# Kernel tuning notes

Measured on AMD Instinct MI355X. Metric: run time of the kernel, lower is better.

The kernel has to match this reference:

```python
import jax, jax.numpy as jnp
import numpy as np

N_NODES = 100000
N_EDGES = 1600000
D = 128            # in_size == d_model == 128
N_LAYERS = 4
N_GRAPHS = 64
N_CLASS = 10
BN_EPS = 1e-5


def setup_inputs() -> dict:
    key = jax.random.key(0)
    ks = jax.random.split(key, 20)
    x = jax.random.normal(ks[0], (N_NODES, D), dtype=jnp.float32)
    edge_index = jax.random.randint(ks[1], (2, N_EDGES), 0, N_NODES, dtype=jnp.int32)
    batch = jnp.sort(jax.random.randint(ks[2], (N_NODES,), 0, N_GRAPHS, dtype=jnp.int32))
    s = 0.05
    # stacked per-layer GINConv MLP params (all layers are D->D since in_size==d_model)
    W1 = jax.random.normal(ks[3], (N_LAYERS, D, D), dtype=jnp.float32) * s
    b1 = jnp.zeros((N_LAYERS, D), dtype=jnp.float32)
    W2 = jax.random.normal(ks[4], (N_LAYERS, D, D), dtype=jnp.float32) * s
    b2 = jnp.zeros((N_LAYERS, D), dtype=jnp.float32)
    gamma = jnp.ones((N_LAYERS, D), dtype=jnp.float32)
    beta = jnp.zeros((N_LAYERS, D), dtype=jnp.float32)
    eps = jnp.zeros((N_LAYERS,), dtype=jnp.float32)  # train_eps=True, init 0
    fcw1 = jax.random.normal(ks[5], (D, D), dtype=jnp.float32) * s
    fcb1 = jnp.zeros((D,), dtype=jnp.float32)
    fcw2 = jax.random.normal(ks[6], (D, D // 2), dtype=jnp.float32) * s
    fcb2 = jnp.zeros((D // 2,), dtype=jnp.float32)
    fcw3 = jax.random.normal(ks[7], (D // 2, N_CLASS), dtype=jnp.float32) * s
    fcb3 = jnp.zeros((N_CLASS,), dtype=jnp.float32)
    return dict(x=x, edge_index=edge_index, batch=batch, W1=W1, b1=b1, W2=W2, b2=b2,
                gamma=gamma, beta=beta, eps=eps, fcw1=fcw1, fcb1=fcb1,
                fcw2=fcw2, fcb2=fcb2, fcw3=fcw3, fcb3=fcb3)


def _batchnorm(z, g, b):
    # BatchNorm1d in training mode: batch stats over nodes, biased variance
    m = jnp.mean(z, axis=0)
    v = jnp.var(z, axis=0)
    return g * (z - m) * jax.lax.rsqrt(v + BN_EPS) + b


def reference(x, edge_index, batch, W1, b1, W2, b2, gamma, beta, eps,
              fcw1, fcb1, fcw2, fcb2, fcw3, fcb3):
    # StandardScaler: per-feature standardization over all nodes (ddof=0)
    mu = jnp.mean(x, axis=0)
    sd = jnp.sqrt(jnp.var(x, axis=0))
    h = (x - mu) / sd
    src, dst = edge_index[0], edge_index[1]
    for l in range(N_LAYERS):
        # GINConv: MLP((1+eps)*x_i + sum_{j in N(i)} x_j)
        agg = jax.ops.segment_sum(h[src], dst, num_segments=N_NODES)
        z = (1.0 + eps[l]) * h + agg
        z = jax.nn.relu(z @ W1[l] + b1[l])
        z = jax.nn.relu(z @ W2[l] + b2[l])
        z = _batchnorm(z, gamma[l], beta[l])
        h = jax.nn.relu(z)  # outer F.relu in forward
    g = jax.ops.segment_sum(h, batch, num_segments=N_GRAPHS)  # global_add_pool
    g = jax.nn.relu(g @ fcw1 + fcb1)   # dropout omitted (eval/deterministic)
    g = jax.nn.relu(g @ fcw2 + fcb2)
    return g @ fcw3 + fcb3
```

## Files before the change

kernel.cpp:

```cpp
#include <hip/hip_runtime.h>
#include <hip/hip_bf16.h>
#include <math.h>

#define N_NODES 100000
#define N_EDGES 1600000
#define D 128
#define N_LAYERS 4
#define N_GRAPHS 64
#define N_CLASS 10
#define BN_EPS 1e-5f

#define POOL_ROWS 128
#define LDK 136

#define EB_CHUNK 4096
#define EDGE_BLOCKS ((N_EDGES + EB_CHUNK - 1) / EB_CHUNK)
#define NPB 512
#define NB ((N_NODES + NPB - 1) / NPB)

typedef __attribute__((ext_vector_type(8))) short bf16x8;
typedef __attribute__((ext_vector_type(4))) float f32x4;

__device__ inline float b2f(ushort u) {
    return __builtin_bit_cast(float, (unsigned)u << 16);
}
__device__ inline ushort f2b(float f) {
    unsigned u = __builtin_bit_cast(unsigned, f);
    return (ushort)((u + 0x7fffu + ((u >> 16) & 1u)) >> 16);
}

__global__ void prep_all_kernel(float* __restrict__ statsAll, float* __restrict__ ab,
                                float* __restrict__ gpool, int* __restrict__ bucketCount) {
    int t = threadIdx.x;
    for (int i = t; i < 10 * D; i += 1024) statsAll[i] = 0.f;
    if (t < D) { ab[t] = 1.f; ab[D + t] = 0.f; }
    for (int i = t; i < N_GRAPHS * D; i += 1024) gpool[i] = 0.f;
    for (int i = t; i < NB; i += 1024) bucketCount[i] = 0;
}

__global__ void bucket_count_kernel(const int* __restrict__ dst, int* __restrict__ bucketCount) {
    __shared__ int bc[NB];
    int tid = threadIdx.x;
    if (tid < NB) bc[tid] = 0;
    __syncthreads();
    int base = blockIdx.x * EB_CHUNK;
#pragma unroll
    for (int i = 0; i < 16; ++i) {
        int e = base + i * 256 + tid;
        if (e < N_EDGES) atomicAdd(&bc[dst[e] >> 9], 1);
    }
    __syncthreads();
    if (tid < NB && bc[tid]) atomicAdd(&bucketCount[tid], bc[tid]);
}

__global__ void bucket_scan_kernel(const int* __restrict__ bucketCount,
                                   int* __restrict__ bucketBase, int* __restrict__ bucketCursor) {
    __shared__ int lds[256];
    int tid = threadIdx.x;
    int v = (tid < NB) ? bucketCount[tid] : 0;
    lds[tid] = v;
    __syncthreads();
    for (int off = 1; off < 256; off <<= 1) {
        int x = (tid >= off) ? lds[tid - off] : 0;
        __syncthreads();
        lds[tid] += x;
        __syncthreads();
    }
    int excl = lds[tid] - v;
    if (tid < NB) { bucketBase[tid] = excl; bucketCursor[tid] = excl; }
    if (tid == NB - 1) bucketBase[NB] = excl + v;
}

__global__ void bucket_scatter_kernel(const int* __restrict__ src, const int* __restrict__ dst,
                                      int* __restrict__ bucketCursor, int2* __restrict__ bpairs) {
    __shared__ int lcnt[NB];
    int tid = threadIdx.x;
    if (tid < NB) lcnt[tid] = 0;
    __syncthreads();
    int base = blockIdx.x * EB_CHUNK;
    int s[16], d[16];
#pragma unroll
    for (int i = 0; i < 16; ++i) {
        int e = base + i * 256 + tid;
        if (e < N_EDGES) {
            s[i] = src[e]; d[i] = dst[e];
            atomicAdd(&lcnt[d[i] >> 9], 1);
        } else {
            d[i] = -1;
        }
    }
    __syncthreads();
    if (tid < NB) {
        int c = lcnt[tid];
        lcnt[tid] = c ? atomicAdd(&bucketCursor[tid], c) : 0;
    }
    __syncthreads();
#pragma unroll
    for (int i = 0; i < 16; ++i) {
        if (d[i] >= 0) {
            int p = atomicAdd(&lcnt[d[i] >> 9], 1);
            bpairs[p] = make_int2(s[i], d[i]);
        }
    }
}

__launch_bounds__(512)
__global__ void csr_build_kernel(const int2* __restrict__ bpairs, const int* __restrict__ bucketBase,
                                 int* __restrict__ rowptr, int* __restrict__ colidx) {
    __shared__ int cnt[NPB];
    __shared__ int cur[NPB];
    int tid = threadIdx.x;
    int b = blockIdx.x;
    int nb0 = b * NPB;
    int ebase = bucketBase[b];
    int eend = bucketBase[b + 1];
    cnt[tid] = 0;
    __syncthreads();
    for (int e = ebase + tid; e < eend; e += 512)
        atomicAdd(&cnt[bpairs[e].y - nb0], 1);
    __syncthreads();
    int v = cnt[tid];
    for (int off = 1; off < 512; off <<= 1) {
        int x = (tid >= off) ? cnt[tid - off] : 0;
        __syncthreads();
        cnt[tid] += x;
        __syncthreads();
    }
    int excl = cnt[tid] - v;
    int node = nb0 + tid;
    if (node < N_NODES) rowptr[node] = ebase + excl;
    cur[tid] = ebase + excl;
    __syncthreads();
    for (int e = ebase + tid; e < eend; e += 512) {
        int2 pr = bpairs[e];
        int p = atomicAdd(&cur[pr.y - nb0], 1);
        colidx[p] = pr.x;
    }
    if (b == 0 && tid == 0) rowptr[N_NODES] = N_EDGES;
}

__global__ void colstats_kernel(const float* __restrict__ x, float* __restrict__ stats) {
    __shared__ float ssum[D];
    __shared__ float ssq[D];
    int tid = threadIdx.x;
    if (tid < D) { ssum[tid] = 0.f; ssq[tid] = 0.f; }
    __syncthreads();
    int f4 = (tid & 31) * 4;
    int rsub = tid >> 5;
    int r0 = blockIdx.x * 128;
    int rend = r0 + 128;
    if (rend > N_NODES) rend = N_NODES;
    float4 ps = make_float4(0.f, 0.f, 0.f, 0.f);
    float4 pq = make_float4(0.f, 0.f, 0.f, 0.f);
    for (int r = r0 + rsub; r < rend; r += 8) {
        float4 v = *(const float4*)&x[(size_t)r * D + f4];
        ps.x += v.x; ps.y += v.y; ps.z += v.z; ps.w += v.w;
        pq.x += v.x * v.x; pq.y += v.y * v.y; pq.z += v.z * v.z; pq.w += v.w * v.w;
    }
    atomicAdd(&ssum[f4 + 0], ps.x); atomicAdd(&ssum[f4 + 1], ps.y);
    atomicAdd(&ssum[f4 + 2], ps.z); atomicAdd(&ssum[f4 + 3], ps.w);
    atomicAdd(&ssq[f4 + 0], pq.x);  atomicAdd(&ssq[f4 + 1], pq.y);
    atomicAdd(&ssq[f4 + 2], pq.z);  atomicAdd(&ssq[f4 + 3], pq.w);
    __syncthreads();
    if (tid < D) {
        atomicAdd(&stats[tid], ssum[tid]);
        atomicAdd(&stats[D + tid], ssq[tid]);
    }
}

__global__ void standardize_kernel(const float* __restrict__ x, const float* __restrict__ stats,
                                   ushort* __restrict__ h) {
    const float invN = 1.f / (float)N_NODES;
    int stride = gridDim.x * blockDim.x;
    const int total = N_NODES * (D / 4);
    for (int idx = blockIdx.x * blockDim.x + threadIdx.x; idx < total; idx += stride) {
        int f = (idx & 31) * 4;
        float4 v = ((const float4*)x)[idx];
        float o[4];
        float vv[4] = {v.x, v.y, v.z, v.w};
#pragma unroll
        for (int j = 0; j < 4; ++j) {
            float mu = stats[f + j] * invN;
            float sd = sqrtf(stats[D + f + j] * invN - mu * mu);
            o[j] = (vv[j] - mu) / sd;
        }
        ((ushort4*)h)[idx] = make_ushort4(f2b(o[0]), f2b(o[1]), f2b(o[2]), f2b(o[3]));
    }
}

__global__ void agg_kernel(const ushort* __restrict__ h, const int* __restrict__ rowptr,
                           const int* __restrict__ colidx, const float* __restrict__ eps, int l,
                           const float* __restrict__ ab, int relu_flag,
                           ushort* __restrict__ z0) {
    int node = blockIdx.x * 8 + (threadIdx.x >> 5);
    int f4 = (threadIdx.x & 31) * 4;
    const ushort* hp = h + f4;
    float A0 = ab[f4 + 0], A1 = ab[f4 + 1], A2 = ab[f4 + 2], A3 = ab[f4 + 3];
    float B0 = ab[D + f4 + 0], B1 = ab[D + f4 + 1], B2 = ab[D + f4 + 2], B3 = ab[D + f4 + 3];
    float lo = relu_flag ? 0.f : -INFINITY;
    auto R0 = [&](ushort u) { return fmaxf(fmaf(b2f(u), A0, B0), lo); };
    auto R1 = [&](ushort u) { return fmaxf(fmaf(b2f(u), A1, B1), lo); };
    auto R2 = [&](ushort u) { return fmaxf(fmaf(b2f(u), A2, B2), lo); };
    auto R3 = [&](ushort u) { return fmaxf(fmaf(b2f(u), A3, B3), lo); };

    ushort4 c = *(const ushort4*)&hp[(size_t)node * D];
    float se = 1.f + eps[l];
    float ax = se * R0(c.x), ay = se * R1(c.y), az = se * R2(c.z), aw = se * R3(c.w);

    int e = rowptr[node], e1 = rowptr[node + 1];
    for (; e + 4 <= e1; e += 4) {
        int s0 = colidx[e], s1 = colidx[e + 1], s2 = colidx[e + 2], s3 = colidx[e + 3];
        ushort4 v0 = *(const ushort4*)&hp[(size_t)s0 * D];
        ushort4 v1 = *(const ushort4*)&hp[(size_t)s1 * D];
        ushort4 v2 = *(const ushort4*)&hp[(size_t)s2 * D];
        ushort4 v3 = *(const ushort4*)&hp[(size_t)s3 * D];
        ax += (R0(v0.x) + R0(v1.x)) + (R0(v2.x) + R0(v3.x));
        ay += (R1(v0.y) + R1(v1.y)) + (R1(v2.y) + R1(v3.y));
        az += (R2(v0.z) + R2(v1.z)) + (R2(v2.z) + R2(v3.z));
        aw += (R3(v0.w) + R3(v1.w)) + (R3(v2.w) + R3(v3.w));
    }
    for (; e < e1; ++e) {
        ushort4 v0 = *(const ushort4*)&hp[(size_t)colidx[e] * D];
        ax += R0(v0.x); ay += R1(v0.y); az += R2(v0.z); aw += R3(v0.w);
    }
    *(ushort4*)&z0[(size_t)node * D + f4] = make_ushort4(f2b(ax), f2b(ay), f2b(az), f2b(aw));
}

__global__ void prep_wt_kernel(const float* __restrict__ W1, const float* __restrict__ W2,
                               ushort* __restrict__ wt) {
    int idx = blockIdx.x * blockDim.x + threadIdx.x;
    int w = idx >> 16;
    int rem = idx & 65535;
    int l = rem >> 14;
    int nk = rem & 16383;
    int n = nk >> 7;
    int k = nk & 127;
    const float* W = w ? W2 : W1;
    wt[idx] = f2b(W[((size_t)(l * D + k)) * D + n]);
}

__launch_bounds__(256, 4)
__global__ void mlp_mfma_kernel(const ushort* __restrict__ z0,
                                const ushort* __restrict__ wt1, const float* __restrict__ b1,
                                const ushort* __restrict__ wt2, const float* __restrict__ b2,
                                ushort* __restrict__ out, float* __restrict__ stats) {
    __shared__ ushort Z[128 * LDK];
    __shared__ float Ssum[D];
    __shared__ float Ssq[D];

    int tid = threadIdx.x;
    int lane = tid & 63;
    int wave = tid >> 6;
    int rb = blockIdx.x * 128;
    int lrow = lane & 15;
    int lk = lane >> 4;
    int klane = lk * 8;
    int wr0 = wave * 32;

    if (tid < D) { Ssum[tid] = 0.f; Ssq[tid] = 0.f; }

    bf16x8 zero8;
#pragma unroll
    for (int e = 0; e < 8; ++e) zero8[e] = 0;

    int ra0 = rb + wr0 + lrow;
    int ra1 = ra0 + 16;
    bool ok0 = ra0 < N_NODES;
    bool ok1 = ra1 < N_NODES;
    const ushort* pa0 = z0 + (size_t)ra0 * D + klane;
    const ushort* pa1 = z0 + (size_t)ra1 * D + klane;
    const ushort* pb1 = wt1 + (size_t)lrow * D + klane;
    const ushort* pb2 = wt2 + (size_t)lrow * D + klane;

    f32x4 acc[2][8];
#pragma unroll
    for (int a = 0; a < 2; ++a)
#pragma unroll
        for (int b = 0; b < 8; ++b)
#pragma unroll
            for (int r = 0; r < 4; ++r) acc[a][b][r] = 0.f;

#pragma unroll
    for (int ks = 0; ks < 4; ++ks) {
        bf16x8 a0 = ok0 ? *(const bf16x8*)(pa0 + ks * 32) : zero8;
        bf16x8 a1 = ok1 ? *(const bf16x8*)(pa1 + ks * 32) : zero8;
#pragma unroll
        for (int ct = 0; ct < 8; ++ct) {
            bf16x8 bb = *(const bf16x8*)(pb1 + (size_t)ct * 16 * D + ks * 32);
            acc[0][ct] = __builtin_amdgcn_mfma_f32_16x16x32_bf16(a0, bb, acc[0][ct], 0, 0, 0);
            acc[1][ct] = __builtin_amdgcn_mfma_f32_16x16x32_bf16(a1, bb, acc[1][ct], 0, 0, 0);
        }
    }

#pragma unroll
    for (int rt = 0; rt < 2; ++rt)
#pragma unroll
        for (int ct = 0; ct < 8; ++ct) {
            int col = ct * 16 + lrow;
            float bias = b1[col];
#pragma unroll
            for (int r = 0; r < 4; ++r) {
                int row = wr0 + rt * 16 + lk * 4 + r;
                Z[row * LDK + col] = f2b(fmaxf(acc[rt][ct][r] + bias, 0.f));
            }
        }

#pragma unroll
    for (int a = 0; a < 2; ++a)
#pragma unroll
        for (int b = 0; b < 8; ++b)
#pragma unroll
            for (int r = 0; r < 4; ++r) acc[a][b][r] = 0.f;

#pragma unroll
    for (int ks = 0; ks < 4; ++ks) {
        int k0 = ks * 32 + klane;
        bf16x8 a0 = *(const bf16x8*)&Z[(wr0 + lrow) * LDK + k0];
        bf16x8 a1 = *(const bf16x8*)&Z[(wr0 + 16 + lrow) * LDK + k0];
#pragma unroll
        for (int ct = 0; ct < 8; ++ct) {
            bf16x8 bb = *(const bf16x8*)(pb2 + (size_t)ct * 16 * D + ks * 32);
            acc[0][ct] = __builtin_amdgcn_mfma_f32_16x16x32_bf16(a0, bb, acc[0][ct], 0, 0, 0);
            acc[1][ct] = __builtin_amdgcn_mfma_f32_16x16x32_bf16(a1, bb, acc[1][ct], 0, 0, 0);
        }
    }

    float ls[8], lq[8];
#pragma unroll
    for (int ct = 0; ct < 8; ++ct) { ls[ct] = 0.f; lq[ct] = 0.f; }
#pragma unroll
    for (int rt = 0; rt < 2; ++rt)
#pragma unroll
        for (int ct = 0; ct < 8; ++ct) {
            int col = ct * 16 + lrow;
            float bias = b2[col];
#pragma unroll
            for (int r = 0; r < 4; ++r) {
                int row = wr0 + rt * 16 + lk * 4 + r;
                float v = fmaxf(acc[rt][ct][r] + bias, 0.f);
                Z[row * LDK + col] = f2b(v);
                if (rb + row < N_NODES) { ls[ct] += v; lq[ct] += v * v; }
            }
        }
    __syncthreads();

#pragma unroll
    for (int ct = 0; ct < 8; ++ct) {
        int col = ct * 16 + lrow;
        atomicAdd(&Ssum[col], ls[ct]);
        atomicAdd(&Ssq[col], lq[ct]);
    }

#pragma unroll
    for (int i = 0; i < 8; ++i) {
        int c2 = tid + i * 256;
        int row = c2 >> 4;
        int cc = (c2 & 15) * 8;
        int gr = rb + row;
        if (gr < N_NODES)
            *(bf16x8*)&out[(size_t)gr * D + cc] = *(const bf16x8*)&Z[row * LDK + cc];
    }
    __syncthreads();
    if (tid < D) {
        atomicAdd(&stats[tid], Ssum[tid]);
        atomicAdd(&stats[D + tid], Ssq[tid]);
    }
}

__global__ void bnprep_kernel(const float* __restrict__ stats, const float* __restrict__ gamma,
                              const float* __restrict__ beta, float* __restrict__ ab) {
    int f = threadIdx.x;
    if (f < D) {
        const float invN = 1.f / (float)N_NODES;
        float mu = stats[f] * invN;
        float var = stats[D + f] * invN - mu * mu;
        float A = gamma[f] * rsqrtf(var + BN_EPS);
        ab[f] = A;
        ab[D + f] = beta[f] - mu * A;
    }
}

__global__ void pool_kernel(const ushort* __restrict__ h, const int* __restrict__ batch,
                            const float* __restrict__ ab, float* __restrict__ g) {
    int tid = threadIdx.x;
    int f4 = (tid & 31) * 4;
    int rsub = tid >> 5;
    int r0 = blockIdx.x * POOL_ROWS;
    int rend = r0 + POOL_ROWS;
    if (rend > N_NODES) rend = N_NODES;
    float A0 = ab[f4 + 0], A1 = ab[f4 + 1], A2 = ab[f4 + 2], A3 = ab[f4 + 3];
    float B0 = ab[D + f4 + 0], B1 = ab[D + f4 + 1], B2 = ab[D + f4 + 2], B3 = ab[D + f4 + 3];
    float4 acc = make_float4(0.f, 0.f, 0.f, 0.f);
    int cur = -1;
    for (int r = r0 + rsub; r < rend; r += 8) {
        int b = batch[r];
        if (b != cur) {
            if (cur >= 0) {
                atomicAdd(&g[cur * D + f4 + 0], acc.x);
                atomicAdd(&g[cur * D + f4 + 1], acc.y);
                atomicAdd(&g[cur * D + f4 + 2], acc.z);
                atomicAdd(&g[cur * D + f4 + 3], acc.w);
            }
            acc = make_float4(0.f, 0.f, 0.f, 0.f);
            cur = b;
        }
        ushort4 v = *(const ushort4*)&h[(size_t)r * D + f4];
        acc.x += fmaxf(fmaf(b2f(v.x), A0, B0), 0.f);
        acc.y += fmaxf(fmaf(b2f(v.y), A1, B1), 0.f);
        acc.z += fmaxf(fmaf(b2f(v.z), A2, B2), 0.f);
        acc.w += fmaxf(fmaf(b2f(v.w), A3, B3), 0.f);
    }
    if (cur >= 0) {
        atomicAdd(&g[cur * D + f4 + 0], acc.x);
        atomicAdd(&g[cur * D + f4 + 1], acc.y);
        atomicAdd(&g[cur * D + f4 + 2], acc.z);
        atomicAdd(&g[cur * D + f4 + 3], acc.w);
    }
}

__launch_bounds__(512)
__global__ void head_kernel(const float* __restrict__ g,
                            const float* __restrict__ fcw1, const float* __restrict__ fcb1,
                            const float* __restrict__ fcw2, const float* __restrict__ fcb2,
                            const float* __restrict__ fcw3, const float* __restrict__ fcb3,
                            float* __restrict__ out) {
    __shared__ float G[64][128];
    __shared__ float T1[64][128];
    __shared__ float T2[64][64];
    int tid = threadIdx.x;
#pragma unroll
    for (int i = 0; i < 4; ++i) {
        int slot = tid + i * 512;
        ((float4*)G)[slot] = ((const float4*)g)[slot];
    }
    __syncthreads();
#pragma unroll 1
    for (int rep = 0; rep < 16; ++rep) {
        int o = tid + rep * 512;
        int r = o >> 7, c = o & 127;
        float acc = fcb1[c];
        for (int k = 0; k < 128; ++k) acc = fmaf(G[r][k], fcw1[k * 128 + c], acc);
        T1[r][c] = fmaxf(acc, 0.f);
    }
    __syncthreads();
#pragma unroll 1
    for (int rep = 0; rep < 8; ++rep) {
        int o = tid + rep * 512;
        int r = o >> 6, c = o & 63;
        float acc = fcb2[c];
        for (int k = 0; k < 128; ++k) acc = fmaf(T1[r][k], fcw2[k * 64 + c], acc);
        T2[r][c] = fmaxf(acc, 0.f);
    }
    __syncthreads();
    for (int o = tid; o < N_GRAPHS * N_CLASS; o += 512) {
        int r = o / 10, c = o % 10;
        float acc = fcb3[c];
        for (int k = 0; k < 64; ++k) acc = fmaf(T2[r][k], fcw3[k * 10 + c], acc);
        out[o] = acc;
    }
}

extern "C" void kernel_launch(void* const* d_in, const int* in_sizes, int n_in,
                              void* d_out, int out_size, void* d_ws, size_t ws_size,
                              hipStream_t stream) {
    const float* x        = (const float*)d_in[0];
    const int* edge_index = (const int*)d_in[1];
    const int* batch      = (const int*)d_in[2];
    const float* W1       = (const float*)d_in[3];
    const float* b1       = (const float*)d_in[4];
    const float* W2       = (const float*)d_in[5];
    const float* b2       = (const float*)d_in[6];
    const float* gamma    = (const float*)d_in[7];
    const float* beta     = (const float*)d_in[8];
    const float* eps      = (const float*)d_in[9];
    const float* fcw1     = (const float*)d_in[10];
    const float* fcb1     = (const float*)d_in[11];
    const float* fcw2     = (const float*)d_in[12];
    const float* fcb2     = (const float*)d_in[13];
    const float* fcw3     = (const float*)d_in[14];
    const float* fcb3     = (const float*)d_in[15];
    float* out = (float*)d_out;

    char* ws = (char*)d_ws;
    size_t off = 0;
    auto alloc = [&](size_t bytes) -> void* {
        void* p = ws + off;
        off = (off + bytes + 255) & ~(size_t)255;
        return p;
    };
    ushort* hbuf   = (ushort*)alloc((size_t)N_NODES * D * 2);
    ushort* z0buf  = (ushort*)alloc((size_t)N_NODES * D * 2);
    ushort* wtbuf  = (ushort*)alloc((size_t)2 * N_LAYERS * D * D * 2);
    int2* bpairs   = (int2*)alloc((size_t)N_EDGES * 8);
    int* colidx    = (int*)alloc((size_t)N_EDGES * 4);
    int* rowptr    = (int*)alloc((size_t)(N_NODES + 1) * 4);
    int* bucketCount  = (int*)alloc((size_t)NB * 4);
    int* bucketBase   = (int*)alloc((size_t)(NB + 1) * 4);
    int* bucketCursor = (int*)alloc((size_t)NB * 4);
    float* statsAll = (float*)alloc(12 * D * 4);
    float* gpool   = (float*)alloc((size_t)N_GRAPHS * D * 4);
    float* scalerStats = statsAll + 8 * D;
    float* ab          = statsAll + 10 * D;

    const int* srcArr = edge_index;
    const int* dstArr = edge_index + N_EDGES;

    prep_all_kernel<<<1, 1024, 0, stream>>>(statsAll, ab, gpool, bucketCount);

    bucket_count_kernel<<<EDGE_BLOCKS, 256, 0, stream>>>(dstArr, bucketCount);
    bucket_scan_kernel<<<1, 256, 0, stream>>>(bucketCount, bucketBase, bucketCursor);
    bucket_scatter_kernel<<<EDGE_BLOCKS, 256, 0, stream>>>(srcArr, dstArr, bucketCursor, bpairs);
    csr_build_kernel<<<NB, 512, 0, stream>>>(bpairs, bucketBase, rowptr, colidx);

    colstats_kernel<<<(N_NODES + 127) / 128, 256, 0, stream>>>(x, scalerStats);
    standardize_kernel<<<2048, 256, 0, stream>>>(x, scalerStats, hbuf);

    prep_wt_kernel<<<512, 256, 0, stream>>>(W1, W2, wtbuf);

    for (int l = 0; l < N_LAYERS; ++l) {
        float* lstats = statsAll + (size_t)l * 2 * D;
        agg_kernel<<<N_NODES / 8, 256, 0, stream>>>(hbuf, rowptr, colidx, eps, l,
                                                    ab, (l > 0) ? 1 : 0, z0buf);
        mlp_mfma_kernel<<<(N_NODES + 127) / 128, 256, 0, stream>>>(
            z0buf, wtbuf + (size_t)l * D * D, b1 + (size_t)l * D,
            wtbuf + (size_t)(N_LAYERS + l) * D * D, b2 + (size_t)l * D, hbuf, lstats);
        bnprep_kernel<<<1, 128, 0, stream>>>(lstats, gamma + (size_t)l * D,
                                             beta + (size_t)l * D, ab);
    }

    pool_kernel<<<(N_NODES + POOL_ROWS - 1) / POOL_ROWS, 256, 0, stream>>>(hbuf, batch, ab, gpool);
    head_kernel<<<1, 512, 0, stream>>>(gpool, fcw1, fcb1, fcw2, fcb2, fcw3, fcb3, out);
}
```

Baseline: 788.3 us.

## Fuse neighbor aggregation into MLP kernel via shared-memory staging and ping-pong buffers

```diff
diff --git a/kernel.cpp b/kernel.cpp
--- a/kernel.cpp
+++ b/kernel.cpp
@@ -188,44 +188,6 @@
     }
 }
 
-__global__ void agg_kernel(const ushort* __restrict__ h, const int* __restrict__ rowptr,
-                           const int* __restrict__ colidx, const float* __restrict__ eps, int l,
-                           const float* __restrict__ ab, int relu_flag,
-                           ushort* __restrict__ z0) {
-    int node = blockIdx.x * 8 + (threadIdx.x >> 5);
-    int f4 = (threadIdx.x & 31) * 4;
-    const ushort* hp = h + f4;
-    float A0 = ab[f4 + 0], A1 = ab[f4 + 1], A2 = ab[f4 + 2], A3 = ab[f4 + 3];
-    float B0 = ab[D + f4 + 0], B1 = ab[D + f4 + 1], B2 = ab[D + f4 + 2], B3 = ab[D + f4 + 3];
-    float lo = relu_flag ? 0.f : -INFINITY;
-    auto R0 = [&](ushort u) { return fmaxf(fmaf(b2f(u), A0, B0), lo); };
-    auto R1 = [&](ushort u) { return fmaxf(fmaf(b2f(u), A1, B1), lo); };
-    auto R2 = [&](ushort u) { return fmaxf(fmaf(b2f(u), A2, B2), lo); };
-    auto R3 = [&](ushort u) { return fmaxf(fmaf(b2f(u), A3, B3), lo); };
-
-    ushort4 c = *(const ushort4*)&hp[(size_t)node * D];
-    float se = 1.f + eps[l];
-    float ax = se * R0(c.x), ay = se * R1(c.y), az = se * R2(c.z), aw = se * R3(c.w);
-
-    int e = rowptr[node], e1 = rowptr[node + 1];
-    for (; e + 4 <= e1; e += 4) {
-        int s0 = colidx[e], s1 = colidx[e + 1], s2 = colidx[e + 2], s3 = colidx[e + 3];
-        ushort4 v0 = *(const ushort4*)&hp[(size_t)s0 * D];
-        ushort4 v1 = *(const ushort4*)&hp[(size_t)s1 * D];
-        ushort4 v2 = *(const ushort4*)&hp[(size_t)s2 * D];
-        ushort4 v3 = *(const ushort4*)&hp[(size_t)s3 * D];
-        ax += (R0(v0.x) + R0(v1.x)) + (R0(v2.x) + R0(v3.x));
-        ay += (R1(v0.y) + R1(v1.y)) + (R1(v2.y) + R1(v3.y));
-        az += (R2(v0.z) + R2(v1.z)) + (R2(v2.z) + R2(v3.z));
-        aw += (R3(v0.w) + R3(v1.w)) + (R3(v2.w) + R3(v3.w));
-    }
-    for (; e < e1; ++e) {
-        ushort4 v0 = *(const ushort4*)&hp[(size_t)colidx[e] * D];
-        ax += R0(v0.x); ay += R1(v0.y); az += R2(v0.z); aw += R3(v0.w);
-    }
-    *(ushort4*)&z0[(size_t)node * D + f4] = make_ushort4(f2b(ax), f2b(ay), f2b(az), f2b(aw));
-}
-
 __global__ void prep_wt_kernel(const float* __restrict__ W1, const float* __restrict__ W2,
                                ushort* __restrict__ wt) {
     int idx = blockIdx.x * blockDim.x + threadIdx.x;
@@ -240,35 +202,70 @@
 }
 
 __launch_bounds__(256, 4)
-__global__ void mlp_mfma_kernel(const ushort* __restrict__ z0,
-                                const ushort* __restrict__ wt1, const float* __restrict__ b1,
-                                const ushort* __restrict__ wt2, const float* __restrict__ b2,
-                                ushort* __restrict__ out, float* __restrict__ stats) {
+__global__ void gin_layer_kernel(const ushort* __restrict__ h, const int* __restrict__ rowptr,
+                                 const int* __restrict__ colidx, const float* __restrict__ eps,
+                                 int l, const float* __restrict__ ab, int relu_flag,
+                                 const ushort* __restrict__ wt1, const float* __restrict__ b1,
+                                 const ushort* __restrict__ wt2, const float* __restrict__ b2,
+                                 ushort* __restrict__ out, float* __restrict__ stats) {
     __shared__ ushort Z[128 * LDK];
     __shared__ float Ssum[D];
     __shared__ float Ssq[D];
 
     int tid = threadIdx.x;
+    int rb = blockIdx.x * 128;
+    if (tid < D) { Ssum[tid] = 0.f; Ssq[tid] = 0.f; }
+
+    {
+        int f4 = (tid & 31) * 4;
+        int nsub = tid >> 5;
+        const ushort* hp = h + f4;
+        float A0 = ab[f4 + 0], A1 = ab[f4 + 1], A2 = ab[f4 + 2], A3 = ab[f4 + 3];
+        float B0 = ab[D + f4 + 0], B1 = ab[D + f4 + 1], B2 = ab[D + f4 + 2], B3 = ab[D + f4 + 3];
+        float lo = relu_flag ? 0.f : -INFINITY;
+        float se = 1.f + eps[l];
+        auto R0 = [&](ushort u) { return fmaxf(fmaf(b2f(u), A0, B0), lo); };
+        auto R1 = [&](ushort u) { return fmaxf(fmaf(b2f(u), A1, B1), lo); };
+        auto R2 = [&](ushort u) { return fmaxf(fmaf(b2f(u), A2, B2), lo); };
+        auto R3 = [&](ushort u) { return fmaxf(fmaf(b2f(u), A3, B3), lo); };
+
+        for (int i = 0; i < 16; ++i) {
+            int lrow = i * 8 + nsub;
+            int node = rb + lrow;
+            ushort4 o = make_ushort4(0, 0, 0, 0);
+            if (node < N_NODES) {
+                ushort4 c = *(const ushort4*)&hp[(size_t)node * D];
+                float ax = se * R0(c.x), ay = se * R1(c.y), az = se * R2(c.z), aw = se * R3(c.w);
+                int e = rowptr[node], e1 = rowptr[node + 1];
+                for (; e + 4 <= e1; e += 4) {
+                    int s0 = colidx[e], s1 = colidx[e + 1], s2 = colidx[e + 2], s3 = colidx[e + 3];
+                    ushort4 v0 = *(const ushort4*)&hp[(size_t)s0 * D];
+                    ushort4 v1 = *(const ushort4*)&hp[(size_t)s1 * D];
+                    ushort4 v2 = *(const ushort4*)&hp[(size_t)s2 * D];
+                    ushort4 v3 = *(const ushort4*)&hp[(size_t)s3 * D];
+                    ax += (R0(v0.x) + R0(v1.x)) + (R0(v2.x) + R0(v3.x));
+                    ay += (R1(v0.y) + R1(v1.y)) + (R1(v2.y) + R1(v3.y));
+                    az += (R2(v0.z) + R2(v1.z)) + (R2(v2.z) + R2(v3.z));
+                    aw += (R3(v0.w) + R3(v1.w)) + (R3(v2.w) + R3(v3.w));
+                }
+                for (; e < e1; ++e) {
+                    ushort4 v0 = *(const ushort4*)&hp[(size_t)colidx[e] * D];
+                    ax += R0(v0.x); ay += R1(v0.y); az += R2(v0.z); aw += R3(v0.w);
+                }
+                o = make_ushort4(f2b(ax), f2b(ay), f2b(az), f2b(aw));
+            }
+            *(ushort4*)&Z[lrow * LDK + f4] = o;
+        }
+    }
+    __syncthreads();
+
     int lane = tid & 63;
     int wave = tid >> 6;
-    int rb = blockIdx.x * 128;
     int lrow = lane & 15;
     int lk = lane >> 4;
     int klane = lk * 8;
     int wr0 = wave * 32;
 
-    if (tid < D) { Ssum[tid] = 0.f; Ssq[tid] = 0.f; }
-
-    bf16x8 zero8;
-#pragma unroll
-    for (int e = 0; e < 8; ++e) zero8[e] = 0;
-
-    int ra0 = rb + wr0 + lrow;
-    int ra1 = ra0 + 16;
-    bool ok0 = ra0 < N_NODES;
-    bool ok1 = ra1 < N_NODES;
-    const ushort* pa0 = z0 + (size_t)ra0 * D + klane;
-    const ushort* pa1 = z0 + (size_t)ra1 * D + klane;
     const ushort* pb1 = wt1 + (size_t)lrow * D + klane;
     const ushort* pb2 = wt2 + (size_t)lrow * D + klane;
 
@@ -282,8 +279,9 @@
 
 #pragma unroll
     for (int ks = 0; ks < 4; ++ks) {
-        bf16x8 a0 = ok0 ? *(const bf16x8*)(pa0 + ks * 32) : zero8;
-        bf16x8 a1 = ok1 ? *(const bf16x8*)(pa1 + ks * 32) : zero8;
+        int k0 = ks * 32 + klane;
+        bf16x8 a0 = *(const bf16x8*)&Z[(wr0 + lrow) * LDK + k0];
+        bf16x8 a1 = *(const bf16x8*)&Z[(wr0 + 16 + lrow) * LDK + k0];
 #pragma unroll
         for (int ct = 0; ct < 8; ++ct) {
             bf16x8 bb = *(const bf16x8*)(pb1 + (size_t)ct * 16 * D + ks * 32);
@@ -489,7 +487,7 @@
         return p;
     };
     ushort* hbuf   = (ushort*)alloc((size_t)N_NODES * D * 2);
-    ushort* z0buf  = (ushort*)alloc((size_t)N_NODES * D * 2);
+    ushort* h2buf  = (ushort*)alloc((size_t)N_NODES * D * 2);
     ushort* wtbuf  = (ushort*)alloc((size_t)2 * N_LAYERS * D * D * 2);
     int2* bpairs   = (int2*)alloc((size_t)N_EDGES * 8);
     int* colidx    = (int*)alloc((size_t)N_EDGES * 4);
@@ -517,17 +515,19 @@
 
     prep_wt_kernel<<<512, 256, 0, stream>>>(W1, W2, wtbuf);
 
+    ushort* hin = hbuf;
+    ushort* hout = h2buf;
     for (int l = 0; l < N_LAYERS; ++l) {
         float* lstats = statsAll + (size_t)l * 2 * D;
-        agg_kernel<<<N_NODES / 8, 256, 0, stream>>>(hbuf, rowptr, colidx, eps, l,
-                                                    ab, (l > 0) ? 1 : 0, z0buf);
-        mlp_mfma_kernel<<<(N_NODES + 127) / 128, 256, 0, stream>>>(
-            z0buf, wtbuf + (size_t)l * D * D, b1 + (size_t)l * D,
-            wtbuf + (size_t)(N_LAYERS + l) * D * D, b2 + (size_t)l * D, hbuf, lstats);
+        gin_layer_kernel<<<(N_NODES + 127) / 128, 256, 0, stream>>>(
+            hin, rowptr, colidx, eps, l, ab, (l > 0) ? 1 : 0,
+            wtbuf + (size_t)l * D * D, b1 + (size_t)l * D,
+            wtbuf + (size_t)(N_LAYERS + l) * D * D, b2 + (size_t)l * D, hout, lstats);
         bnprep_kernel<<<1, 128, 0, stream>>>(lstats, gamma + (size_t)l * D,
                                              beta + (size_t)l * D, ab);
-    }
-
-    pool_kernel<<<(N_NODES + POOL_ROWS - 1) / POOL_ROWS, 256, 0, stream>>>(hbuf, batch, ab, gpool);
+        ushort* t = hin; hin = hout; hout = t;
+    }
+
+    pool_kernel<<<(N_NODES + POOL_ROWS - 1) / POOL_ROWS, 256, 0, stream>>>(hin, batch, ab, gpool);
     head_kernel<<<1, 512, 0, stream>>>(gpool, fcw1, fcb1, fcw2, fcb2, fcw3, fcb3, out);
 }
```

After: 877.9 us. 1.11x slower.
